# Performance work log

Hardware: AMD Instinct MI355X
Metric: run time of the kernel (lower is better)

The kernel has to match this reference:

```python
import jax, jax.numpy as jnp
import numpy as np

IN_CH = 64
OUT_CH = 64
K = 5
PAD = 2
B, H, W = 16, 128, 128


def _build_buffers():
    # Mirrors the torch __init__ geometry construction exactly.
    r = (K - 1) // 2
    x = np.arange(-r, r + 1)
    X = np.stack(np.meshgrid(x, x, indexing='ij'), -1).astype(np.float32)  # (K,K,2)
    R = np.sqrt((X ** 2).sum(-1))                                          # (K,K)
    with np.errstate(divide='ignore', invalid='ignore'):
        Xhat = X / R[..., None]
    Xhat[R == 0] = 0.0
    Xhat = np.transpose(Xhat, (2, 0, 1))                 # (2,K,K)
    XX = Xhat[None, :] * Xhat[:, None]                   # (2,2,K,K) outer product
    XX = np.tile(XX, (OUT_CH, IN_CH, 1, 1))              # (2*out, 2*in, K, K)
    rs, inds = np.unique(R, return_inverse=True)
    inds = inds.reshape(K, K).astype(np.int32)
    indsxx = inds - 1
    indsxx[indsxx == -1] = 0                              # r=0 bin has no xx term (masked by XX=0 there)
    identity = np.tile(np.eye(2, dtype=np.float32), (OUT_CH, IN_CH))[..., None, None]  # (2*out,2*in,1,1)
    return XX.astype(np.float32), identity, indsxx, inds, len(rs)


def setup_inputs() -> dict:
    XX, identity, indsxx, indsid, L = _build_buffers()
    key = jax.random.key(0)
    k1, k2, k3 = jax.random.split(key, 3)
    scale = np.float32(1.0 / np.sqrt(3 * IN_CH * 2))
    return {
        'x': jax.random.normal(k1, (B, 2 * IN_CH, H, W), jnp.float32),
        'weightsxx': jax.random.normal(k2, (OUT_CH, IN_CH, L - 1), jnp.float32) * scale,
        'weightsidentity': jax.random.normal(k3, (OUT_CH, IN_CH, L), jnp.float32) * scale,
        'XhatXhat': jnp.asarray(XX),
        'identity': jnp.asarray(identity),
        'indsxx': jnp.asarray(indsxx),
        'indsidentity': jnp.asarray(indsid),
        'padding': PAD,
    }


def _build_kernel(weightsxx, weightsidentity, XhatXhat, identity, indsxx, indsidentity):
    # repeat_interleave(.,2,axis) == jnp.repeat(.,2,axis); then radial gather over (K,K)
    cxx = jnp.repeat(jnp.repeat(weightsxx, 2, axis=0), 2, axis=1)[..., indsxx] * XhatXhat
    cid = jnp.repeat(jnp.repeat(weightsidentity, 2, axis=0), 2, axis=1)[..., indsidentity] * identity
    return cxx + cid  # (2*out, 2*in, K, K)


def reference(x, weightsxx, weightsidentity, XhatXhat, identity, indsxx, indsidentity, padding):
    c = _build_kernel(weightsxx, weightsidentity, XhatXhat, identity, indsxx, indsidentity)
    xp = jnp.pad(x, ((0, 0), (0, 0), (padding, padding), (padding, padding)))
    return jax.lax.conv_general_dilated(
        xp, c, window_strides=(1, 1), padding='VALID',
        dimension_numbers=('NCHW', 'OIHW', 'NCHW'))
```

## Files before the change

### kernel.cpp

```cpp
#include <hip/hip_runtime.h>
#include <hip/hip_bf16.h>
#include <utility>

typedef __bf16        bf16x8 __attribute__((ext_vector_type(8)));
typedef float         f32x16 __attribute__((ext_vector_type(16)));
typedef unsigned int  u32x4  __attribute__((ext_vector_type(4)));
typedef unsigned int   u32;
typedef unsigned short u16;

template<int N> using IC = std::integral_constant<int, N>;

__device__ __forceinline__ u16 f32_to_bf16(float f) {
    u32 u = __builtin_bit_cast(u32, f);
    u = (u + 0x7FFFu + ((u >> 16) & 1u)) >> 16;
    return (u16)u;
}
__device__ __forceinline__ u32 pack2bf(float a, float b) {
    return (u32)f32_to_bf16(a) | ((u32)f32_to_bf16(b) << 16);
}

__global__ void build_c(const float* __restrict__ wxx,
                        const float* __restrict__ wid,
                        const float* __restrict__ XX,
                        const float* __restrict__ ident,
                        const int*   __restrict__ indsxx,
                        const int*   __restrict__ indsid,
                        u16*         __restrict__ cb)
{
    int idx = blockIdx.x * 256 + threadIdx.x;
    if (idx >= 25 * 128 * 128) return;
    int b = idx & 127;
    int a = (idx >> 7) & 127;
    int t = idx >> 14;
    int w2 = (a >> 1) * 64 + (b >> 1);
    float v = wxx[w2 * 5 + indsxx[t]] * XX[(a * 128 + b) * 25 + t]
            + ident[a * 128 + b]      * wid[w2 * 6 + indsid[t]];
    cb[idx] = f32_to_bf16(v);
}

constexpr int LDSROW = 68 * 48;
constexpr int LDSBUF = 8 * LDSROW;

__global__ void __launch_bounds__(256, 2)
conv_mfma(const float* __restrict__ x,
          const u16*   __restrict__ cb,
          float*       __restrict__ out)
{
    __shared__ unsigned char lds[2 * LDSBUF];

    const int tid    = threadIdx.x;
    const int lane   = tid & 63;
    const int wv     = tid >> 6;
    const int wave_m = wv & 1;
    const int wave_q = wv >> 1;
    const int l31    = lane & 31;
    const int h2     = lane >> 5;

    const int bid  = blockIdx.x;
    const int sbid = (bid & 7) * 128 + (bid >> 3);
    const int bb   = sbid >> 6;
    const int tile = sbid & 63;
    const int h0   = (tile >> 1) << 2;
    const int w0   = (tile & 1) << 6;

    const int wc  = tid & 63;
    const int ic8 = (tid >> 6) & 1;
    const int rh  = tid >> 7;

    const int hsel  = tid & 3;
    const int wcolH = (hsel < 2) ? (hsel - 2) : (62 + hsel);
    const int ic8H  = (tid >> 2) & 1;
    const int rH    = tid >> 3;
    const int hIdxH = wcolH + 2;

    f32x16 acc[2][4];
    #pragma unroll
    for (int i = 0; i < 2; ++i)
        #pragma unroll
        for (int j = 0; j < 4; ++j)
            #pragma unroll
            for (int k = 0; k < 16; ++k) acc[i][j][k] = 0.f;

    float pf[4][8];
    float pfh[8];

    const float* xbase = x + (size_t)bb * (128 * 16384);
    const u16*   cbA0  = cb + (wave_m * 64 + l31) * 128 + h2 * 8;

    auto ISSUE = [&](auto Uc, int s) {
        constexpr int U = decltype(Uc)::value;
        const int hp = h0 - 2 + 2 * U + rh;
        if ((unsigned)hp < 128u) {
            const float* px = xbase + (size_t)(s * 16 + ic8 * 8) * 16384 + hp * 128 + w0 + wc;
            #pragma unroll
            for (int j = 0; j < 8; ++j) pf[U][j] = px[(size_t)j * 16384];
        } else {
            #pragma unroll
            for (int j = 0; j < 8; ++j) pf[U][j] = 0.f;
        }
    };

    auto ISSUEH = [&](int s) {
        if (tid < 64) {
            const int hp = h0 - 2 + rH;
            const int gc = w0 + wcolH;
            if ((unsigned)hp < 128u && (unsigned)gc < 128u) {
                const float* px = xbase + (size_t)(s * 16 + ic8H * 8) * 16384 + hp * 128 + gc;
                #pragma unroll
                for (int j = 0; j < 8; ++j) pfh[j] = px[(size_t)j * 16384];
            } else {
                #pragma unroll
                for (int j = 0; j < 8; ++j) pfh[j] = 0.f;
            }
        }
    };

    auto WRITE = [&](auto Uc, int wbuf) {
        constexpr int U = decltype(Uc)::value;
        u32x4 v;
        v[0] = pack2bf(pf[U][0], pf[U][1]);
        v[1] = pack2bf(pf[U][2], pf[U][3]);
        v[2] = pack2bf(pf[U][4], pf[U][5]);
        v[3] = pack2bf(pf[U][6], pf[U][7]);
        *reinterpret_cast<u32x4*>(&lds[wbuf * LDSBUF + (2 * U + rh) * LDSROW
                                       + (wc + 2) * 48 + ic8 * 16]) = v;
    };

    auto WRITEH = [&](int wbuf) {
        if (tid < 64) {
            u32x4 v;
            v[0] = pack2bf(pfh[0], pfh[1]);
            v[1] = pack2bf(pfh[2], pfh[3]);
            v[2] = pack2bf(pfh[4], pfh[5]);
            v[3] = pack2bf(pfh[6], pfh[7]);
            *reinterpret_cast<u32x4*>(&lds[wbuf * LDSBUF + rH * LDSROW
                                           + hIdxH * 48 + ic8H * 16]) = v;
        }
    };

    auto CLUSTER = [&](auto KWc, int s) {
        constexpr int KW = decltype(KWc)::value;
        const u16* abase = cbA0 + KW * 16384 + s * 16;
        bf16x8 A[5][2];
        #pragma unroll
        for (int kh = 0; kh < 5; ++kh) {
            A[kh][0] = *reinterpret_cast<const bf16x8*>(abase + kh * 81920);
            A[kh][1] = *reinterpret_cast<const bf16x8*>(abase + kh * 81920 + 4096);
        }
        const unsigned char* lbase = &lds[(s & 1) * LDSBUF
                                          + (wave_q * 32 + l31 + KW) * 48 + h2 * 16];
        __builtin_amdgcn_s_setprio(1);
        #pragma unroll
        for (int rp = 0; rp < 8; ++rp) {
            const bf16x8 b = *reinterpret_cast<const bf16x8*>(lbase + rp * LDSROW);
            #pragma unroll
            for (int kh = 0; kh < 5; ++kh) {
                const int n = rp - kh;
                if (0 <= n && n < 4) {
                    acc[0][n] = __builtin_amdgcn_mfma_f32_32x32x16_bf16(A[kh][0], b, acc[0][n], 0, 0, 0);
                    acc[1][n] = __builtin_amdgcn_mfma_f32_32x32x16_bf16(A[kh][1], b, acc[1][n], 0, 0, 0);
                }
            }
        }
        __builtin_amdgcn_s_setprio(0);
    };

    ISSUE(IC<0>{}, 0); ISSUE(IC<1>{}, 0); ISSUE(IC<2>{}, 0); ISSUE(IC<3>{}, 0); ISSUEH(0);
    WRITE(IC<0>{}, 0); WRITE(IC<1>{}, 0); WRITE(IC<2>{}, 0); WRITE(IC<3>{}, 0); WRITEH(0);
    __syncthreads();

    #pragma unroll 1
    for (int s = 0; s < 8; ++s) {
        const int nb = (s + 1) & 1;
        if (s < 7) {
            ISSUE(IC<0>{}, s + 1); ISSUE(IC<1>{}, s + 1);
            ISSUE(IC<2>{}, s + 1); ISSUE(IC<3>{}, s + 1); ISSUEH(s + 1);
        }
        CLUSTER(IC<0>{}, s);
        if (s < 7) WRITE(IC<0>{}, nb);
        CLUSTER(IC<1>{}, s);
        if (s < 7) WRITE(IC<1>{}, nb);
        CLUSTER(IC<2>{}, s);
        if (s < 7) WRITE(IC<2>{}, nb);
        CLUSTER(IC<3>{}, s);
        if (s < 7) { WRITE(IC<3>{}, nb); WRITEH(nb); }
        CLUSTER(IC<4>{}, s);
        __syncthreads();
    }

    const int wpix = w0 + wave_q * 32 + l31;
    #pragma unroll
    for (int m = 0; m < 2; ++m)
        #pragma unroll
        for (int reg = 0; reg < 16; ++reg) {
            const int oc = wave_m * 64 + m * 32 + (reg & 3) + ((reg >> 2) << 3) + (h2 << 2);
            float* op = out + ((size_t)(bb * 128 + oc) * 128 + h0) * 128 + wpix;
            #pragma unroll
            for (int n = 0; n < 4; ++n)
                op[n * 128] = acc[m][n][reg];
        }
}

extern "C" void kernel_launch(void* const* d_in, const int* in_sizes, int n_in,
                              void* d_out, int out_size, void* d_ws, size_t ws_size,
                              hipStream_t stream)
{
    const float* x    = (const float*)d_in[0];
    const float* wxx  = (const float*)d_in[1];
    const float* wi   = (const float*)d_in[2];
    const float* XX   = (const float*)d_in[3];
    const float* iden = (const float*)d_in[4];
    const int*   ixx  = (const int*)d_in[5];
    const int*   iid  = (const int*)d_in[6];

    u16* cbuf = (u16*)d_ws;

    build_c<<<1600, 256, 0, stream>>>(wxx, wi, XX, iden, ixx, iid, cbuf);
    conv_mfma<<<1024, 256, 0, stream>>>(x, cbuf, (float*)d_out);
}
```

Before: 245.9 us.

## Split output channels across blocks and software-pipeline weight loads across kw clusters

```diff
diff --git a/kernel.cpp b/kernel.cpp
--- a/kernel.cpp
+++ b/kernel.cpp
@@ -56,16 +56,19 @@
     const int l31    = lane & 31;
     const int h2     = lane >> 5;
 
-    const int bid  = blockIdx.x;
-    const int sbid = (bid & 7) * 128 + (bid >> 3);
-    const int bb   = sbid >> 6;
-    const int tile = sbid & 63;
-    const int h0   = (tile >> 1) << 2;
-    const int w0   = (tile & 1) << 6;
+    const int bid = blockIdx.x;
+    const int swz = (bid & 7) * 256 + (bid >> 3);
+    const int bo  = swz & 1;
+    const int wq  = (swz >> 1) & 1;
+    const int ht  = (swz >> 2) & 31;
+    const int bb  = swz >> 7;
+    const int h0  = ht << 2;
+    const int w0  = wq << 6;
+    const int ocb = bo << 6;
 
     const int wc  = tid & 63;
     const int ic8 = (tid >> 6) & 1;
-    const int rh  = tid >> 7;
+    const int rh  = (tid >> 7) & 1;
 
     const int hsel  = tid & 3;
     const int wcolH = (hsel < 2) ? (hsel - 2) : (62 + hsel);
@@ -73,19 +76,27 @@
     const int rH    = tid >> 3;
     const int hIdxH = wcolH + 2;
 
-    f32x16 acc[2][4];
+    f32x16 acc[4];
     #pragma unroll
-    for (int i = 0; i < 2; ++i)
-        #pragma unroll
-        for (int j = 0; j < 4; ++j)
-            #pragma unroll
-            for (int k = 0; k < 16; ++k) acc[i][j][k] = 0.f;
-
-    float pf[4][8];
-    float pfh[8];
+    for (int j = 0; j < 4; ++j)
+        #pragma unroll
+        for (int k = 0; k < 16; ++k) acc[j][k] = 0.f;
+
+    float  pf[4][8];
+    float  pfh[8];
+    bf16x8 A[2][5];
 
     const float* xbase = x + (size_t)bb * (128 * 16384);
-    const u16*   cbA0  = cb + (wave_m * 64 + l31) * 128 + h2 * 8;
+    const u16*   cbA0  = cb + (ocb + wave_m * 32 + l31) * 128 + h2 * 8;
+
+    auto ALOAD = [&](auto Pc, auto KWc, int s) {
+        constexpr int P  = decltype(Pc)::value;
+        constexpr int KW = decltype(KWc)::value;
+        const u16* ab = cbA0 + KW * 16384 + s * 16;
+        #pragma unroll
+        for (int kh = 0; kh < 5; ++kh)
+            A[P][kh] = *reinterpret_cast<const bf16x8*>(ab + kh * 81920);
+    };
 
     auto ISSUE = [&](auto Uc, int s) {
         constexpr int U = decltype(Uc)::value;
@@ -115,39 +126,36 @@
         }
     };
 
-    auto WRITE = [&](auto Uc, int wbuf) {
-        constexpr int U = decltype(Uc)::value;
+    auto WRITE = [&](auto Uc, auto WBc) {
+        constexpr int U  = decltype(Uc)::value;
+        constexpr int WB = decltype(WBc)::value;
         u32x4 v;
         v[0] = pack2bf(pf[U][0], pf[U][1]);
         v[1] = pack2bf(pf[U][2], pf[U][3]);
         v[2] = pack2bf(pf[U][4], pf[U][5]);
         v[3] = pack2bf(pf[U][6], pf[U][7]);
-        *reinterpret_cast<u32x4*>(&lds[wbuf * LDSBUF + (2 * U + rh) * LDSROW
+        *reinterpret_cast<u32x4*>(&lds[WB * LDSBUF + (2 * U + rh) * LDSROW
                                        + (wc + 2) * 48 + ic8 * 16]) = v;
     };
 
-    auto WRITEH = [&](int wbuf) {
+    auto WRITEH = [&](auto WBc) {
+        constexpr int WB = decltype(WBc)::value;
         if (tid < 64) {
             u32x4 v;
             v[0] = pack2bf(pfh[0], pfh[1]);
             v[1] = pack2bf(pfh[2], pfh[3]);
             v[2] = pack2bf(pfh[4], pfh[5]);
             v[3] = pack2bf(pfh[6], pfh[7]);
-            *reinterpret_cast<u32x4*>(&lds[wbuf * LDSBUF + rH * LDSROW
+            *reinterpret_cast<u32x4*>(&lds[WB * LDSBUF + rH * LDSROW
                                            + hIdxH * 48 + ic8H * 16]) = v;
         }
     };
 
-    auto CLUSTER = [&](auto KWc, int s) {
+    auto COMPUTE = [&](auto Pc, auto KWc, auto RBc) {
+        constexpr int P  = decltype(Pc)::value;
         constexpr int KW = decltype(KWc)::value;
-        const u16* abase = cbA0 + KW * 16384 + s * 16;
-        bf16x8 A[5][2];
-        #pragma unroll
-        for (int kh = 0; kh < 5; ++kh) {
-            A[kh][0] = *reinterpret_cast<const bf16x8*>(abase + kh * 81920);
-            A[kh][1] = *reinterpret_cast<const bf16x8*>(abase + kh * 81920 + 4096);
-        }
-        const unsigned char* lbase = &lds[(s & 1) * LDSBUF
+        constexpr int RB = decltype(RBc)::value;
+        const unsigned char* lbase = &lds[RB * LDSBUF
                                           + (wave_q * 32 + l31 + KW) * 48 + h2 * 16];
         __builtin_amdgcn_s_setprio(1);
         #pragma unroll
@@ -156,49 +164,66 @@
             #pragma unroll
             for (int kh = 0; kh < 5; ++kh) {
                 const int n = rp - kh;
-                if (0 <= n && n < 4) {
-                    acc[0][n] = __builtin_amdgcn_mfma_f32_32x32x16_bf16(A[kh][0], b, acc[0][n], 0, 0, 0);
-                    acc[1][n] = __builtin_amdgcn_mfma_f32_32x32x16_bf16(A[kh][1], b, acc[1][n], 0, 0, 0);
-                }
+                if (0 <= n && n < 4)
+                    acc[n] = __builtin_amdgcn_mfma_f32_32x32x16_bf16(A[P][kh], b, acc[n], 0, 0, 0);
             }
         }
         __builtin_amdgcn_s_setprio(0);
     };
 
+    auto SBAR = [&]() {
+        asm volatile("s_waitcnt lgkmcnt(0)" ::: "memory");
+        __builtin_amdgcn_s_barrier();
+        __builtin_amdgcn_sched_barrier(0);
+    };
+
     ISSUE(IC<0>{}, 0); ISSUE(IC<1>{}, 0); ISSUE(IC<2>{}, 0); ISSUE(IC<3>{}, 0); ISSUEH(0);
-    WRITE(IC<0>{}, 0); WRITE(IC<1>{}, 0); WRITE(IC<2>{}, 0); WRITE(IC<3>{}, 0); WRITEH(0);
+    WRITE(IC<0>{}, IC<0>{}); WRITE(IC<1>{}, IC<0>{});
+    WRITE(IC<2>{}, IC<0>{}); WRITE(IC<3>{}, IC<0>{}); WRITEH(IC<0>{});
+    ALOAD(IC<0>{}, IC<0>{}, 0);
     __syncthreads();
 
+    auto STAGE = [&](auto SPc, int s) {
+        constexpr int SP = decltype(SPc)::value;
+        constexpr int RB = SP;
+        constexpr int WB = SP ^ 1;
+        const bool pfon = (s < 7);
+        ALOAD(IC<(1 + SP) & 1>{}, IC<1>{}, s);
+        if (pfon) ISSUE(IC<0>{}, s + 1);
+        COMPUTE(IC<SP>{}, IC<0>{}, IC<RB>{});
+        ALOAD(IC<SP>{}, IC<2>{}, s);
+        if (pfon) ISSUE(IC<1>{}, s + 1);
+        COMPUTE(IC<(1 + SP) & 1>{}, IC<1>{}, IC<RB>{});
+        if (pfon) WRITE(IC<0>{}, IC<WB>{});
+        ALOAD(IC<(1 + SP) & 1>{}, IC<3>{}, s);
+        if (pfon) ISSUE(IC<2>{}, s + 1);
+        COMPUTE(IC<SP>{}, IC<2>{}, IC<RB>{});
+        if (pfon) WRITE(IC<1>{}, IC<WB>{});
+        ALOAD(IC<SP>{}, IC<4>{}, s);
+        if (pfon) { ISSUE(IC<3>{}, s + 1); ISSUEH(s + 1); }
+        COMPUTE(IC<(1 + SP) & 1>{}, IC<3>{}, IC<RB>{});
+        if (pfon) WRITE(IC<2>{}, IC<WB>{});
+        if (pfon) ALOAD(IC<(1 + SP) & 1>{}, IC<0>{}, s + 1);
+        COMPUTE(IC<SP>{}, IC<4>{}, IC<RB>{});
+        if (pfon) { WRITE(IC<3>{}, IC<WB>{}); WRITEH(IC<WB>{}); }
+        SBAR();
+    };
+
     #pragma unroll 1
-    for (int s = 0; s < 8; ++s) {
-        const int nb = (s + 1) & 1;
-        if (s < 7) {
-            ISSUE(IC<0>{}, s + 1); ISSUE(IC<1>{}, s + 1);
-            ISSUE(IC<2>{}, s + 1); ISSUE(IC<3>{}, s + 1); ISSUEH(s + 1);
-        }
-        CLUSTER(IC<0>{}, s);
-        if (s < 7) WRITE(IC<0>{}, nb);
-        CLUSTER(IC<1>{}, s);
-        if (s < 7) WRITE(IC<1>{}, nb);
-        CLUSTER(IC<2>{}, s);
-        if (s < 7) WRITE(IC<2>{}, nb);
-        CLUSTER(IC<3>{}, s);
-        if (s < 7) { WRITE(IC<3>{}, nb); WRITEH(nb); }
-        CLUSTER(IC<4>{}, s);
-        __syncthreads();
+    for (int sp = 0; sp < 4; ++sp) {
+        STAGE(IC<0>{}, 2 * sp);
+        STAGE(IC<1>{}, 2 * sp + 1);
     }
 
     const int wpix = w0 + wave_q * 32 + l31;
     #pragma unroll
-    for (int m = 0; m < 2; ++m)
-        #pragma unroll
-        for (int reg = 0; reg < 16; ++reg) {
-            const int oc = wave_m * 64 + m * 32 + (reg & 3) + ((reg >> 2) << 3) + (h2 << 2);
-            float* op = out + ((size_t)(bb * 128 + oc) * 128 + h0) * 128 + wpix;
-            #pragma unroll
-            for (int n = 0; n < 4; ++n)
-                op[n * 128] = acc[m][n][reg];
-        }
+    for (int reg = 0; reg < 16; ++reg) {
+        const int oc = ocb + wave_m * 32 + (reg & 3) + ((reg >> 2) << 3) + (h2 << 2);
+        float* op = out + ((size_t)(bb * 128 + oc) * 128 + h0) * 128 + wpix;
+        #pragma unroll
+        for (int n = 0; n < 4; ++n)
+            op[n * 128] = acc[n][reg];
+    }
 }
 
 extern "C" void kernel_launch(void* const* d_in, const int* in_sizes, int n_in,
@@ -216,5 +241,5 @@
     u16* cbuf = (u16*)d_ws;
 
     build_c<<<1600, 256, 0, stream>>>(wxx, wi, XX, iden, ixx, iid, cbuf);
-    conv_mfma<<<1024, 256, 0, stream>>>(x, cbuf, (float*)d_out);
-}
+    conv_mfma<<<2048, 256, 0, stream>>>(x, cbuf, (float*)d_out);
+}
```

Result: no change. 250.2 us (+1.7%).

## Pre-transpose input to padded bf16 layout and stream tiles via global_load_lds

Applied to the files above, without the earlier changes.

```diff
diff --git a/kernel.cpp b/kernel.cpp
--- a/kernel.cpp
+++ b/kernel.cpp
@@ -38,15 +38,40 @@
     cb[idx] = f32_to_bf16(v);
 }
 
-constexpr int LDSROW = 68 * 48;
-constexpr int LDSBUF = 8 * LDSROW;
+__global__ void transpose_pad(const float* __restrict__ x, u16* __restrict__ xT)
+{
+    int idx = blockIdx.x * 256 + threadIdx.x;
+    if (idx >= 16 * 8 * 132 * 264) return;
+    int c2 = idx % 264;
+    int h1 = (idx / 264) % 132;
+    int s  = (idx / (264 * 132)) % 8;
+    int b  = idx / (264 * 132 * 8);
+    int wp = c2 >> 1, half = c2 & 1;
+    int h = h1 - 2, w = wp - 2;
+    u32x4 v = {0u, 0u, 0u, 0u};
+    if ((unsigned)h < 128u && (unsigned)w < 128u) {
+        const float* px = x + (((size_t)(b * 128 + s * 16 + half * 8)) * 128 + h) * 128 + w;
+        float f[8];
+        #pragma unroll
+        for (int i = 0; i < 8; ++i) f[i] = px[(size_t)i * 16384];
+        v[0] = pack2bf(f[0], f[1]); v[1] = pack2bf(f[2], f[3]);
+        v[2] = pack2bf(f[4], f[5]); v[3] = pack2bf(f[6], f[7]);
+    }
+    *reinterpret_cast<u32x4*>(xT + (size_t)idx * 8) = v;
+}
+
+constexpr int ROWB = 68 * 32;
+constexpr int BUFB = 8 * ROWB;
+constexpr int GROW = 132 * 32;
+constexpr int GSPL = 132 * GROW;
+constexpr int GB   = 8 * GSPL;
 
 __global__ void __launch_bounds__(256, 2)
-conv_mfma(const float* __restrict__ x,
-          const u16*   __restrict__ cb,
-          float*       __restrict__ out)
-{
-    __shared__ unsigned char lds[2 * LDSBUF];
+conv_mfma(const u16* __restrict__ xT,
+          const u16* __restrict__ cb,
+          float*     __restrict__ out)
+{
+    __shared__ unsigned char lds[2 * BUFB];
 
     const int tid    = threadIdx.x;
     const int lane   = tid & 63;
@@ -63,15 +88,136 @@
     const int h0   = (tile >> 1) << 2;
     const int w0   = (tile & 1) << 6;
 
-    const int wc  = tid & 63;
-    const int ic8 = (tid >> 6) & 1;
-    const int rh  = tid >> 7;
-
-    const int hsel  = tid & 3;
+    const int j0 = (wv == 0) ? 0 : (wv * 4 + 1);
+    const int nj = (wv == 0) ? 5 : 4;
+    unsigned go[5];
+    #pragma unroll
+    for (int jj = 0; jj < 5; ++jj) {
+        const int off = (j0 + jj) * 1024 + lane * 16;
+        const int r   = off / ROWB;
+        go[jj] = (unsigned)(r * GROW + (off - r * ROWB));
+    }
+    const char* xTb = (const char*)xT + (size_t)bb * GB + (size_t)h0 * GROW + (size_t)w0 * 32;
+
+    auto DMA = [&](int s, int wbuf) {
+        const char* sb = xTb + (size_t)s * GSPL;
+        #pragma unroll
+        for (int jj = 0; jj < 5; ++jj) {
+            if (jj < nj) {
+                __builtin_amdgcn_global_load_lds(
+                    (const __attribute__((address_space(1))) u32*)(sb + go[jj]),
+                    (__attribute__((address_space(3))) u32*)(lds + wbuf * BUFB + (j0 + jj) * 1024),
+                    16, 0, 0);
+            }
+        }
+    };
+
+    f32x16 acc[2][4];
+    #pragma unroll
+    for (int i = 0; i < 2; ++i)
+        #pragma unroll
+        for (int j = 0; j < 4; ++j)
+            #pragma unroll
+            for (int k = 0; k < 16; ++k) acc[i][j][k] = 0.f;
+
+    bf16x8 A[2][5][2];
+    const u16* cbA0 = cb + (wave_m * 64 + l31) * 128 + h2 * 8;
+
+    auto ALOAD = [&](auto Pc, int kw, int s) {
+        constexpr int P = decltype(Pc)::value;
+        const u16* ab = cbA0 + kw * 16384 + s * 16;
+        #pragma unroll
+        for (int kh = 0; kh < 5; ++kh) {
+            A[P][kh][0] = *reinterpret_cast<const bf16x8*>(ab + kh * 81920);
+            A[P][kh][1] = *reinterpret_cast<const bf16x8*>(ab + kh * 81920 + 4096);
+        }
+    };
+
+    auto COMPUTE = [&](auto Pc, auto KWc, auto RBc) {
+        constexpr int P  = decltype(Pc)::value;
+        constexpr int KW = decltype(KWc)::value;
+        constexpr int RB = decltype(RBc)::value;
+        const unsigned char* lb = &lds[RB * BUFB + (wave_q * 32 + l31 + KW) * 32 + h2 * 16];
+        __builtin_amdgcn_s_setprio(1);
+        #pragma unroll
+        for (int rp = 0; rp < 8; ++rp) {
+            const bf16x8 b = *reinterpret_cast<const bf16x8*>(lb + rp * ROWB);
+            #pragma unroll
+            for (int kh = 0; kh < 5; ++kh) {
+                const int n = rp - kh;
+                if (0 <= n && n < 4) {
+                    acc[0][n] = __builtin_amdgcn_mfma_f32_32x32x16_bf16(A[P][kh][0], b, acc[0][n], 0, 0, 0);
+                    acc[1][n] = __builtin_amdgcn_mfma_f32_32x32x16_bf16(A[P][kh][1], b, acc[1][n], 0, 0, 0);
+                }
+            }
+        }
+        __builtin_amdgcn_s_setprio(0);
+    };
+
+    DMA(0, 0);
+    ALOAD(IC<0>{}, 0, 0);
+    asm volatile("s_waitcnt vmcnt(0)" ::: "memory");
+    __builtin_amdgcn_s_barrier();
+    __builtin_amdgcn_sched_barrier(0);
+
+    auto STAGE = [&](auto SPc, int s) {
+        constexpr int SP = decltype(SPc)::value;
+        constexpr int OP = SP ^ 1;
+        const bool pfon = (s < 7);
+        if (pfon) DMA(s + 1, OP);
+        ALOAD(IC<OP>{}, 1, s);
+        COMPUTE(IC<SP>{}, IC<0>{}, IC<SP>{});
+        ALOAD(IC<SP>{}, 2, s);
+        COMPUTE(IC<OP>{}, IC<1>{}, IC<SP>{});
+        ALOAD(IC<OP>{}, 3, s);
+        COMPUTE(IC<SP>{}, IC<2>{}, IC<SP>{});
+        ALOAD(IC<SP>{}, 4, s);
+        COMPUTE(IC<OP>{}, IC<3>{}, IC<SP>{});
+        if (pfon) ALOAD(IC<OP>{}, 0, s + 1);
+        COMPUTE(IC<SP>{}, IC<4>{}, IC<SP>{});
+        asm volatile("s_waitcnt vmcnt(0) lgkmcnt(0)" ::: "memory");
+        __builtin_amdgcn_s_barrier();
+        __builtin_amdgcn_sched_barrier(0);
+    };
+
+    #pragma unroll 1
+    for (int sp = 0; sp < 4; ++sp) {
+        STAGE(IC<0>{}, 2 * sp);
+        STAGE(IC<1>{}, 2 * sp + 1);
+    }
+
+    const int wpix = w0 + wave_q * 32 + l31;
+    #pragma unroll
+    for (int m = 0; m < 2; ++m)
+        #pragma unroll
+        for (int reg = 0; reg < 16; ++reg) {
+            const int oc = wave_m * 64 + m * 32 + (reg & 3) + ((reg >> 2) << 3) + (h2 << 2);
+            float* op = out + ((size_t)(bb * 128 + oc) * 128 + h0) * 128 + wpix;
+            #pragma unroll
+            for (int n = 0; n < 4; ++n)
+                op[n * 128] = acc[m][n][reg];
+        }
+}
+
+constexpr int FROW = 68 * 48;
+constexpr int FBUF = 8 * FROW;
+
+__global__ void __launch_bounds__(256, 2)
+conv_mfma_fb(const float* __restrict__ x,
+             const u16*   __restrict__ cb,
+             float*       __restrict__ out)
+{
+    __shared__ unsigned char lds[2 * FBUF];
+    const int tid = threadIdx.x, lane = tid & 63, wv = tid >> 6;
+    const int wave_m = wv & 1, wave_q = wv >> 1, l31 = lane & 31, h2 = lane >> 5;
+    const int bid = blockIdx.x;
+    const int sbid = (bid & 7) * 128 + (bid >> 3);
+    const int bb = sbid >> 6, tile = sbid & 63;
+    const int h0 = (tile >> 1) << 2, w0 = (tile & 1) << 6;
+    const int wc = tid & 63, ic8 = (tid >> 6) & 1, rh = (tid >> 7) & 1;
+    const int hsel = tid & 3;
     const int wcolH = (hsel < 2) ? (hsel - 2) : (62 + hsel);
-    const int ic8H  = (tid >> 2) & 1;
-    const int rH    = tid >> 3;
-    const int hIdxH = wcolH + 2;
+    const int ic8H = (tid >> 2) & 1, rH = tid >> 3, hIdxH = wcolH + 2;
 
     f32x16 acc[2][4];
     #pragma unroll
@@ -81,11 +227,9 @@
             #pragma unroll
             for (int k = 0; k < 16; ++k) acc[i][j][k] = 0.f;
 
-    float pf[4][8];
-    float pfh[8];
-
+    float pf[4][8]; float pfh[8];
     const float* xbase = x + (size_t)bb * (128 * 16384);
-    const u16*   cbA0  = cb + (wave_m * 64 + l31) * 128 + h2 * 8;
+    const u16* cbA0 = cb + (wave_m * 64 + l31) * 128 + h2 * 8;
 
     auto ISSUE = [&](auto Uc, int s) {
         constexpr int U = decltype(Uc)::value;
@@ -99,11 +243,9 @@
             for (int j = 0; j < 8; ++j) pf[U][j] = 0.f;
         }
     };
-
     auto ISSUEH = [&](int s) {
         if (tid < 64) {
-            const int hp = h0 - 2 + rH;
-            const int gc = w0 + wcolH;
+            const int hp = h0 - 2 + rH, gc = w0 + wcolH;
             if ((unsigned)hp < 128u && (unsigned)gc < 128u) {
                 const float* px = xbase + (size_t)(s * 16 + ic8H * 8) * 16384 + hp * 128 + gc;
                 #pragma unroll
@@ -114,30 +256,21 @@
             }
         }
     };
-
     auto WRITE = [&](auto Uc, int wbuf) {
         constexpr int U = decltype(Uc)::value;
         u32x4 v;
-        v[0] = pack2bf(pf[U][0], pf[U][1]);
-        v[1] = pack2bf(pf[U][2], pf[U][3]);
-        v[2] = pack2bf(pf[U][4], pf[U][5]);
-        v[3] = pack2bf(pf[U][6], pf[U][7]);
-        *reinterpret_cast<u32x4*>(&lds[wbuf * LDSBUF + (2 * U + rh) * LDSROW
-                                       + (wc + 2) * 48 + ic8 * 16]) = v;
-    };
-
+        v[0] = pack2bf(pf[U][0], pf[U][1]); v[1] = pack2bf(pf[U][2], pf[U][3]);
+        v[2] = pack2bf(pf[U][4], pf[U][5]); v[3] = pack2bf(pf[U][6], pf[U][7]);
+        *reinterpret_cast<u32x4*>(&lds[wbuf * FBUF + (2 * U + rh) * FROW + (wc + 2) * 48 + ic8 * 16]) = v;
+    };
     auto WRITEH = [&](int wbuf) {
         if (tid < 64) {
             u32x4 v;
-            v[0] = pack2bf(pfh[0], pfh[1]);
-            v[1] = pack2bf(pfh[2], pfh[3]);
-            v[2] = pack2bf(pfh[4], pfh[5]);
-            v[3] = pack2bf(pfh[6], pfh[7]);
-            *reinterpret_cast<u32x4*>(&lds[wbuf * LDSBUF + rH * LDSROW
-                                           + hIdxH * 48 + ic8H * 16]) = v;
-        }
-    };
-
+            v[0] = pack2bf(pfh[0], pfh[1]); v[1] = pack2bf(pfh[2], pfh[3]);
+            v[2] = pack2bf(pfh[4], pfh[5]); v[3] = pack2bf(pfh[6], pfh[7]);
+            *reinterpret_cast<u32x4*>(&lds[wbuf * FBUF + rH * FROW + hIdxH * 48 + ic8H * 16]) = v;
+        }
+    };
     auto CLUSTER = [&](auto KWc, int s) {
         constexpr int KW = decltype(KWc)::value;
         const u16* abase = cbA0 + KW * 16384 + s * 16;
@@ -147,12 +280,11 @@
             A[kh][0] = *reinterpret_cast<const bf16x8*>(abase + kh * 81920);
             A[kh][1] = *reinterpret_cast<const bf16x8*>(abase + kh * 81920 + 4096);
         }
-        const unsigned char* lbase = &lds[(s & 1) * LDSBUF
-                                          + (wave_q * 32 + l31 + KW) * 48 + h2 * 16];
+        const unsigned char* lb = &lds[(s & 1) * FBUF + (wave_q * 32 + l31 + KW) * 48 + h2 * 16];
         __builtin_amdgcn_s_setprio(1);
         #pragma unroll
         for (int rp = 0; rp < 8; ++rp) {
-            const bf16x8 b = *reinterpret_cast<const bf16x8*>(lbase + rp * LDSROW);
+            const bf16x8 b = *reinterpret_cast<const bf16x8*>(lb + rp * FROW);
             #pragma unroll
             for (int kh = 0; kh < 5; ++kh) {
                 const int n = rp - kh;
@@ -213,8 +345,18 @@
     const int*   ixx  = (const int*)d_in[5];
     const int*   iid  = (const int*)d_in[6];
 
-    u16* cbuf = (u16*)d_ws;
-
-    build_c<<<1600, 256, 0, stream>>>(wxx, wi, XX, iden, ixx, iid, cbuf);
-    conv_mfma<<<1024, 256, 0, stream>>>(x, cbuf, (float*)d_out);
-}
+    const size_t XT_BYTES = 71368704ull;
+    const size_t NEED     = XT_BYTES + 819200ull;
+
+    if (ws_size >= NEED) {
+        u16* xTb  = (u16*)d_ws;
+        u16* cbuf = (u16*)((char*)d_ws + XT_BYTES);
+        build_c<<<1600, 256, 0, stream>>>(wxx, wi, XX, iden, ixx, iid, cbuf);
+        transpose_pad<<<17424, 256, 0, stream>>>(x, xTb);
+        conv_mfma<<<1024, 256, 0, stream>>>(xTb, cbuf, (float*)d_out);
+    } else {
+        u16* cbuf = (u16*)d_ws;
+        build_c<<<1600, 256, 0, stream>>>(wxx, wi, XX, iden, ixx, iid, cbuf);
+        conv_mfma_fb<<<1024, 256, 0, stream>>>(x, cbuf, (float*)d_out);
+    }
+}
```

Result: slower. 328.0 us (+33.4%).

## Split output channels across two blocks to halve accumulators and raise occupancy

Applied to the files above, without the earlier changes.

```diff
diff --git a/kernel.cpp b/kernel.cpp
--- a/kernel.cpp
+++ b/kernel.cpp
@@ -41,7 +41,7 @@
 constexpr int LDSROW = 68 * 48;
 constexpr int LDSBUF = 8 * LDSROW;
 
-__global__ void __launch_bounds__(256, 2)
+__global__ void __launch_bounds__(256, 3)
 conv_mfma(const float* __restrict__ x,
           const u16*   __restrict__ cb,
           float*       __restrict__ out)
@@ -56,16 +56,19 @@
     const int l31    = lane & 31;
     const int h2     = lane >> 5;
 
-    const int bid  = blockIdx.x;
-    const int sbid = (bid & 7) * 128 + (bid >> 3);
-    const int bb   = sbid >> 6;
-    const int tile = sbid & 63;
-    const int h0   = (tile >> 1) << 2;
-    const int w0   = (tile & 1) << 6;
+    const int bid = blockIdx.x;
+    const int swz = (bid & 7) * 256 + (bid >> 3);
+    const int g   = swz & 1;
+    const int wt  = (swz >> 1) & 1;
+    const int ht  = (swz >> 2) & 31;
+    const int bb  = swz >> 7;
+    const int h0  = ht << 2;
+    const int w0  = wt << 6;
+    const int ocb = g << 6;
 
     const int wc  = tid & 63;
     const int ic8 = (tid >> 6) & 1;
-    const int rh  = tid >> 7;
+    const int rh  = (tid >> 7) & 1;
 
     const int hsel  = tid & 3;
     const int wcolH = (hsel < 2) ? (hsel - 2) : (62 + hsel);
@@ -73,19 +76,17 @@
     const int rH    = tid >> 3;
     const int hIdxH = wcolH + 2;
 
-    f32x16 acc[2][4];
+    f32x16 acc[4];
     #pragma unroll
-    for (int i = 0; i < 2; ++i)
-        #pragma unroll
-        for (int j = 0; j < 4; ++j)
-            #pragma unroll
-            for (int k = 0; k < 16; ++k) acc[i][j][k] = 0.f;
+    for (int j = 0; j < 4; ++j)
+        #pragma unroll
+        for (int k = 0; k < 16; ++k) acc[j][k] = 0.f;
 
     float pf[4][8];
     float pfh[8];
 
     const float* xbase = x + (size_t)bb * (128 * 16384);
-    const u16*   cbA0  = cb + (wave_m * 64 + l31) * 128 + h2 * 8;
+    const u16*   cbA0  = cb + (ocb + wave_m * 32 + l31) * 128 + h2 * 8;
 
     auto ISSUE = [&](auto Uc, int s) {
         constexpr int U = decltype(Uc)::value;
@@ -141,25 +142,21 @@
     auto CLUSTER = [&](auto KWc, int s) {
         constexpr int KW = decltype(KWc)::value;
         const u16* abase = cbA0 + KW * 16384 + s * 16;
-        bf16x8 A[5][2];
-        #pragma unroll
-        for (int kh = 0; kh < 5; ++kh) {
-            A[kh][0] = *reinterpret_cast<const bf16x8*>(abase + kh * 81920);
-            A[kh][1] = *reinterpret_cast<const bf16x8*>(abase + kh * 81920 + 4096);
-        }
-        const unsigned char* lbase = &lds[(s & 1) * LDSBUF
-                                          + (wave_q * 32 + l31 + KW) * 48 + h2 * 16];
+        bf16x8 A[5];
+        #pragma unroll
+        for (int kh = 0; kh < 5; ++kh)
+            A[kh] = *reinterpret_cast<const bf16x8*>(abase + kh * 81920);
+        const unsigned char* lb = &lds[(s & 1) * LDSBUF
+                                       + (wave_q * 32 + l31 + KW) * 48 + h2 * 16];
         __builtin_amdgcn_s_setprio(1);
         #pragma unroll
         for (int rp = 0; rp < 8; ++rp) {
-            const bf16x8 b = *reinterpret_cast<const bf16x8*>(lbase + rp * LDSROW);
+            const bf16x8 b = *reinterpret_cast<const bf16x8*>(lb + rp * LDSROW);
             #pragma unroll
             for (int kh = 0; kh < 5; ++kh) {
                 const int n = rp - kh;
-                if (0 <= n && n < 4) {
-                    acc[0][n] = __builtin_amdgcn_mfma_f32_32x32x16_bf16(A[kh][0], b, acc[0][n], 0, 0, 0);
-                    acc[1][n] = __builtin_amdgcn_mfma_f32_32x32x16_bf16(A[kh][1], b, acc[1][n], 0, 0, 0);
-                }
+                if (0 <= n && n < 4)
+                    acc[n] = __builtin_amdgcn_mfma_f32_32x32x16_bf16(A[kh], b, acc[n], 0, 0, 0);
             }
         }
         __builtin_amdgcn_s_setprio(0);
@@ -190,15 +187,13 @@
 
     const int wpix = w0 + wave_q * 32 + l31;
     #pragma unroll
-    for (int m = 0; m < 2; ++m)
-        #pragma unroll
-        for (int reg = 0; reg < 16; ++reg) {
-            const int oc = wave_m * 64 + m * 32 + (reg & 3) + ((reg >> 2) << 3) + (h2 << 2);
-            float* op = out + ((size_t)(bb * 128 + oc) * 128 + h0) * 128 + wpix;
-            #pragma unroll
-            for (int n = 0; n < 4; ++n)
-                op[n * 128] = acc[m][n][reg];
-        }
+    for (int reg = 0; reg < 16; ++reg) {
+        const int oc = ocb + wave_m * 32 + (reg & 3) + ((reg >> 2) << 3) + (h2 << 2);
+        float* op = out + ((size_t)(bb * 128 + oc) * 128 + h0) * 128 + wpix;
+        #pragma unroll
+        for (int n = 0; n < 4; ++n)
+            op[n * 128] = acc[n][reg];
+    }
 }
 
 extern "C" void kernel_launch(void* const* d_in, const int* in_sizes, int n_in,
@@ -216,5 +211,5 @@
     u16* cbuf = (u16*)d_ws;
 
     build_c<<<1600, 256, 0, stream>>>(wxx, wi, XX, iden, ixx, iid, cbuf);
-    conv_mfma<<<1024, 256, 0, stream>>>(x, cbuf, (float*)d_out);
-}
+    conv_mfma<<<2048, 256, 0, stream>>>(x, cbuf, (float*)d_out);
+}
```

Result: slower. 255.7 us (+4.0%).
